# Kernel optimization log

Hardware: AMD Instinct MI355X
Metric: run time of the kernel (lower is better)

## Reference

```python
import jax, jax.numpy as jnp
import numpy as np

D = 512
H = 8
HD = D // H

def setup_inputs() -> dict:
    key = jax.random.key(0)
    ks = jax.random.split(key, 16)
    B, L = 8, 384
    s = 1.0 / np.sqrt(D)
    inp = {
        "hidden_states": jax.random.normal(ks[0], (B, L, D), jnp.float32),
        "position_embeddings": jax.random.normal(ks[1], (L, L, D), jnp.float32),
        "attention_mask": jnp.ones((B, L), jnp.int32),
        "ln_g": jnp.ones((D,), jnp.float32),
        "ln_b": jnp.zeros((D,), jnp.float32),
        "Wq": jax.random.normal(ks[2], (D, D), jnp.float32) * s,
        "bq": jnp.zeros((D,), jnp.float32),
        "Wk": jax.random.normal(ks[3], (D, D), jnp.float32) * s,
        "bk": jnp.zeros((D,), jnp.float32),
        "Wv": jax.random.normal(ks[4], (D, D), jnp.float32) * s,
        "bv": jnp.zeros((D,), jnp.float32),
        "Wpos": jax.random.normal(ks[5], (D, D), jnp.float32) * s,
        "pos_bias_u": jax.random.normal(ks[6], (H, HD), jnp.float32) * 0.02,
        "pos_bias_v": jax.random.normal(ks[7], (H, HD), jnp.float32) * 0.02,
        "Wo": jax.random.normal(ks[8], (D, D), jnp.float32) * s,
        "bo": jnp.zeros((D,), jnp.float32),
    }
    return inp

def _layernorm(x, g, b, eps=1e-5):
    mu = jnp.mean(x, axis=-1, keepdims=True)
    var = jnp.var(x, axis=-1, keepdims=True)
    return (x - mu) * jax.lax.rsqrt(var + eps) * g + b

def reference(hidden_states, position_embeddings, attention_mask,
              ln_g, ln_b, Wq, bq, Wk, bk, Wv, bv, Wpos,
              pos_bias_u, pos_bias_v, Wo, bo):
    B, L, _ = hidden_states.shape
    x = _layernorm(hidden_states, ln_g, ln_b)
    # projections -> (B, L, H, HD)
    q = (x @ Wq.T + bq).reshape(B, L, H, HD)
    k = (x @ Wk.T + bk).reshape(B, L, H, HD)
    v = (x @ Wv.T + bv).reshape(B, L, H, HD)
    # relative position projection -> (H, L, L, HD); pos[h, i, j, d]
    pos = (position_embeddings @ Wpos.T).reshape(L, L, H, HD)
    pos = jnp.transpose(pos, (2, 0, 1, 3))
    q_u = q + pos_bias_u  # (B, L, H, HD)
    q_v = q + pos_bias_v
    # content score: ac[b,h,i,j] = sum_d q_u[b,i,h,d] * k[b,j,h,d]
    scores_ac = jnp.einsum('bihd,bjhd->bhij', q_u, k)
    # positional score (torch broadcast semantics): bd[b,h,i,j] = sum_d q_v[b,j,h,d] * pos[h,i,j,d]
    scores_bd = jnp.einsum('bjhd,hijd->bhij', q_v, pos)
    scores = (scores_ac + scores_bd) / np.sqrt(HD)
    mask = attention_mask[:, None, None, :]  # (B,1,1,L)
    scores = jnp.where(mask == 0, jnp.finfo(scores.dtype).min, scores)
    probs = jax.nn.softmax(scores, axis=-1)
    ctx = jnp.einsum('bhij,bjhd->bihd', probs, v).reshape(B, L, D)
    return ctx @ Wo.T + bo
```

## Files before the change

### kernel.cpp

```cpp
#include <hip/hip_runtime.h>
#include <hip/hip_bf16.h>

#define DEV __device__ __forceinline__

typedef short short8 __attribute__((ext_vector_type(8)));
typedef float f32x4 __attribute__((ext_vector_type(4)));
typedef unsigned short ushort4v __attribute__((ext_vector_type(4)));
typedef unsigned short u16;

DEV u16 f2b(float x){ __hip_bfloat16 h = __float2bfloat16(x); u16 u; __builtin_memcpy(&u, &h, 2); return u; }

DEV int swz(int row, int cb){ return row*128 + (cb ^ ((row & 7) << 4)); }
DEV int swz768(int row, int byte_in_row){ return row*768 + (byte_in_row ^ ((row & 7) << 4)); }

DEV short8 ldfrag(const u16* s, int row, int kbf){
  return *(const short8*)((const char*)s + swz(row, kbf*2));
}
DEV void st16(u16* s, int row, int cb, short8 v){
  *(short8*)((char*)s + swz(row, cb)) = v;
}
DEV f32x4 MFMA(short8 a, short8 b, f32x4 c){
  return __builtin_amdgcn_mfma_f32_16x16x32_bf16(a, b, c, 0, 0, 0);
}

template<int R>
DEV void stage_bf16(u16* lds, const u16* g, size_t rstride, int tid){
  #pragma unroll
  for (int c = tid; c < R*8; c += 256){
    int row = c >> 3, k = c & 7;
    short8 v = *(const short8*)(g + (size_t)row*rstride + k*8);
    st16(lds, row, k*16, v);
  }
}

template<int R>
DEV void stage_f32(u16* lds, const float* g, size_t rstride, int tid){
  #pragma unroll
  for (int c = tid; c < R*8; c += 256){
    int row = c >> 3, k = c & 7;
    const float* p = g + (size_t)row*rstride + k*8;
    f32x4 f0 = *(const f32x4*)p;
    f32x4 f1 = *(const f32x4*)(p + 4);
    short8 v;
    #pragma unroll
    for (int t = 0; t < 4; ++t){ v[t] = (short)f2b(f0[t]); v[t+4] = (short)f2b(f1[t]); }
    st16(lds, row, k*16, v);
  }
}

template<int MI, int NI>
DEV void mma_step(const u16* As, int ar0, const u16* Bs, int br0, f32x4 (&acc)[MI][NI], int lane){
  int r = lane & 15, kb = (lane >> 4) * 8;
  #pragma unroll
  for (int kk = 0; kk < 64; kk += 32){
    short8 a[MI], b[NI];
    #pragma unroll
    for (int mi = 0; mi < MI; ++mi) a[mi] = ldfrag(As, ar0 + mi*16 + r, kk + kb);
    #pragma unroll
    for (int ni = 0; ni < NI; ++ni) b[ni] = ldfrag(Bs, br0 + ni*16 + r, kk + kb);
    #pragma unroll
    for (int mi = 0; mi < MI; ++mi)
      #pragma unroll
      for (int ni = 0; ni < NI; ++ni)
        acc[mi][ni] = MFMA(a[mi], b[ni], acc[mi][ni]);
  }
}

__global__ __launch_bounds__(256) void k_ln(const float* __restrict__ hs, const float* __restrict__ g,
                                            const float* __restrict__ bb, u16* __restrict__ xbf){
  int lane = threadIdx.x & 63, wid = threadIdx.x >> 6;
  int row = blockIdx.x * 4 + wid;
  const float* p = hs + (size_t)row * 512;
  f32x4 v0 = ((const f32x4*)p)[lane];
  f32x4 v1 = ((const f32x4*)p)[lane + 64];
  float s = 0.f, s2 = 0.f;
  #pragma unroll
  for (int t = 0; t < 4; ++t){ s += v0[t] + v1[t]; s2 += v0[t]*v0[t] + v1[t]*v1[t]; }
  #pragma unroll
  for (int off = 32; off; off >>= 1){ s += __shfl_xor(s, off); s2 += __shfl_xor(s2, off); }
  float mu = s * (1.0f/512.0f);
  float var = s2 * (1.0f/512.0f) - mu*mu;
  float rs = rsqrtf(var + 1e-5f);
  int e0 = lane * 4, e1 = 256 + e0;
  ushort4v o0, o1;
  #pragma unroll
  for (int t = 0; t < 4; ++t){
    o0[t] = f2b((v0[t]-mu)*rs*g[e0+t]+bb[e0+t]);
    o1[t] = f2b((v1[t]-mu)*rs*g[e1+t]+bb[e1+t]);
  }
  *(ushort4v*)(xbf + (size_t)row*512 + e0) = o0;
  *(ushort4v*)(xbf + (size_t)row*512 + e1) = o1;
}

__global__ __launch_bounds__(256) void k_wpt(const float* __restrict__ Wpos, u16* __restrict__ Wpt){
  int idx = blockIdx.x * 256 + threadIdx.x;
  int o = idx >> 9, e = idx & 511;
  int h = o >> 6, d = o & 63;
  Wpt[((size_t)h*512 + e)*64 + d] = f2b(Wpos[idx]);
}

__global__ __launch_bounds__(256) void k_qkv(const u16* __restrict__ xbf,
    const float* __restrict__ Wq, const float* __restrict__ Wk, const float* __restrict__ Wv,
    const float* __restrict__ bq, const float* __restrict__ bk, const float* __restrict__ bv,
    const float* __restrict__ pbu, const float* __restrict__ pbv,
    u16* __restrict__ qu, u16* __restrict__ qv, u16* __restrict__ kkb, u16* __restrict__ vt){
  __shared__ __align__(16) u16 As[128*64];
  __shared__ __align__(16) u16 Bs[128*64];
  int tid = threadIdx.x, lane = tid & 63, wid = tid >> 6;
  int t0 = blockIdx.x * 128, n0 = blockIdx.y * 128, z = blockIdx.z;
  const float* W    = (z==0) ? Wq : (z==1) ? Wk : Wv;
  const float* bias = (z==0) ? bq : (z==1) ? bk : bv;
  f32x4 acc[4][4] = {};
  for (int k0 = 0; k0 < 512; k0 += 64){
    stage_bf16<128>(As, xbf + (size_t)t0*512 + k0, 512, tid);
    stage_f32<128>(Bs, W + (size_t)n0*512 + k0, 512, tid);
    __syncthreads();
    mma_step<4,4>(As, (wid>>1)*64, Bs, (wid&1)*64, acc, lane);
    __syncthreads();
  }
  int r = lane & 15, half = lane >> 4;
  #pragma unroll
  for (int mi = 0; mi < 4; ++mi)
  #pragma unroll
  for (int ni = 0; ni < 4; ++ni){
    int n = n0 + (wid&1)*64 + ni*16 + r;
    int h = n >> 6, d = n & 63;
    int m0 = t0 + (wid>>1)*64 + mi*16 + half*4;
    #pragma unroll
    for (int q = 0; q < 4; ++q){
      int t = m0 + q, b = t / 384, i = t - b*384;
      float v = acc[mi][ni][q] + bias[n];
      if (z == 0){
        qu[((size_t)(b*8+h)*384 + i)*64 + d] = f2b(v + pbu[n]);
        qv[((size_t)h*3072 + t)*64 + d]      = f2b(v + pbv[n]);
      } else if (z == 1){
        kkb[((size_t)(b*8+h)*384 + i)*64 + d] = f2b(v);
      } else {
        vt[((size_t)(b*8+h)*64 + d)*384 + i] = f2b(v);
      }
    }
  }
}

__global__ __launch_bounds__(256) void k_qw(const u16* __restrict__ qv, const u16* __restrict__ Wpt,
                                            u16* __restrict__ qW){
  __shared__ __align__(16) u16 As[128*64];
  __shared__ __align__(16) u16 Bs[128*64];
  int tid = threadIdx.x, lane = tid & 63, wid = tid >> 6;
  int t0 = blockIdx.x * 128, e0 = blockIdx.y * 128, h = blockIdx.z;
  f32x4 acc[4][4] = {};
  stage_bf16<128>(As, qv + ((size_t)h*3072 + t0)*64, 64, tid);
  stage_bf16<128>(Bs, Wpt + ((size_t)h*512 + e0)*64, 64, tid);
  __syncthreads();
  mma_step<4,4>(As, (wid>>1)*64, Bs, (wid&1)*64, acc, lane);
  int r = lane & 15, half = lane >> 4;
  #pragma unroll
  for (int mi = 0; mi < 4; ++mi)
  #pragma unroll
  for (int ni = 0; ni < 4; ++ni){
    int e = e0 + (wid&1)*64 + ni*16 + r;
    int m0 = t0 + (wid>>1)*64 + mi*16 + half*4;
    #pragma unroll
    for (int q = 0; q < 4; ++q){
      int t = m0 + q, b = t / 384, j = t - b*384;
      int bh = b*8 + h;
      qW[((size_t)bh*384 + j)*512 + e] = f2b(acc[mi][ni][q]);
    }
  }
}

__global__ __launch_bounds__(256) void k_bd(const u16* __restrict__ qW, const float* __restrict__ P,
                                            float* __restrict__ Sbd){
  __shared__ __align__(16) u16 As[64*64];
  __shared__ __align__(16) u16 Bs[192*64];
  int tid = threadIdx.x, lane = tid & 63, wid = tid >> 6;
  int j = blockIdx.x, ib = blockIdx.y * 192;
  const u16*  Ag = qW + (size_t)j*512;
  const float* Bg = P + ((size_t)ib*384 + j)*512;
  short8 ar[2];
  f32x4  br[6][2];
  f32x4 acc[4][3] = {};

  #pragma unroll
  for (int s = 0; s < 2; ++s){ int c = tid + s*256;
    ar[s] = *(const short8*)(Ag + (size_t)(c>>3)*(384*512) + (c&7)*8); }
  #pragma unroll
  for (int s = 0; s < 6; ++s){ int c = tid + s*256;
    const float* p = Bg + (size_t)(c>>3)*(384*512) + (c&7)*8;
    br[s][0] = *(const f32x4*)p; br[s][1] = *(const f32x4*)(p+4); }

  #pragma unroll
  for (int k0 = 0; k0 < 512; k0 += 64){
    #pragma unroll
    for (int s = 0; s < 2; ++s){ int c = tid + s*256; st16(As, c>>3, (c&7)*16, ar[s]); }
    #pragma unroll
    for (int s = 0; s < 6; ++s){ int c = tid + s*256;
      short8 v;
      #pragma unroll
      for (int t = 0; t < 4; ++t){ v[t] = (short)f2b(br[s][0][t]); v[t+4] = (short)f2b(br[s][1][t]); }
      st16(Bs, c>>3, (c&7)*16, v); }
    if (k0 + 64 < 512){
      #pragma unroll
      for (int s = 0; s < 2; ++s){ int c = tid + s*256;
        ar[s] = *(const short8*)(Ag + (size_t)(c>>3)*(384*512) + (k0+64) + (c&7)*8); }
      #pragma unroll
      for (int s = 0; s < 6; ++s){ int c = tid + s*256;
        const float* p = Bg + (size_t)(c>>3)*(384*512) + (k0+64) + (c&7)*8;
        br[s][0] = *(const f32x4*)p; br[s][1] = *(const f32x4*)(p+4); }
    }
    __syncthreads();
    mma_step<4,3>(As, 0, Bs, wid*48, acc, lane);
    __syncthreads();
  }
  int r = lane & 15, half = lane >> 4;
  #pragma unroll
  for (int mi = 0; mi < 4; ++mi)
  #pragma unroll
  for (int ni = 0; ni < 3; ++ni){
    int i = ib + wid*48 + ni*16 + r;
    #pragma unroll
    for (int q = 0; q < 4; ++q){
      int bh = mi*16 + half*4 + q;
      Sbd[((size_t)j*64 + bh)*384 + i] = acc[mi][ni][q];
    }
  }
}

__global__ __launch_bounds__(256) void k_fin(const u16* __restrict__ qu, const u16* __restrict__ kkb,
                                             const u16* __restrict__ vt, const float* __restrict__ Sbd,
                                             const int* __restrict__ mask, u16* __restrict__ ctx){
  __shared__ __align__(16) char lds[72*1024];
  __shared__ float smbuf[2][4][2][16];
  u16* Ks = (u16*)lds;
  u16* Qs = (u16*)(lds + 48*1024);
  u16* Ps = (u16*)lds;
  u16* Vs = (u16*)(lds + 24*1024);
  int tid = threadIdx.x, lane = tid & 63, wid = tid >> 6;
  int r = lane & 15, half = lane >> 4;
  int i0 = blockIdx.x * 32, bh = blockIdx.y, b = bh >> 3, h = bh & 7;

  stage_bf16<384>(Ks, kkb + (size_t)bh*384*64, 64, tid);
  stage_bf16<32>(Qs, qu + ((size_t)bh*384 + i0)*64, 64, tid);
  __syncthreads();

  f32x4 acc[6][2] = {};
  mma_step<6,2>(Ks, wid*96, Qs, 0, acc, lane);

  int jw = wid*96 + half*4;
  #pragma unroll
  for (int mi = 0; mi < 6; ++mi){
    #pragma unroll
    for (int q = 0; q < 4; ++q){
      int j = jw + mi*16 + q;
      bool dead = (mask[b*384 + j] == 0);
      const float* srow = Sbd + ((size_t)j*64 + bh)*384 + i0;
      #pragma unroll
      for (int ni = 0; ni < 2; ++ni){
        float v = (acc[mi][ni][q] + srow[ni*16 + r]) * 0.125f;
        acc[mi][ni][q] = dead ? -3.402823466e38f : v;
      }
    }
  }

  short8 vreg[12];
  #pragma unroll
  for (int c = 0; c < 12; ++c){
    int cc = tid + c*256;
    int d = cc / 48, jc = cc - d*48;
    vreg[c] = *(const short8*)(vt + ((size_t)bh*64 + d)*384 + jc*8);
  }

  float mx[2];
  #pragma unroll
  for (int ni = 0; ni < 2; ++ni){
    float m = -3.402823466e38f;
    #pragma unroll
    for (int mi = 0; mi < 6; ++mi){
      f32x4 a = acc[mi][ni];
      m = fmaxf(m, fmaxf(fmaxf(a[0],a[1]), fmaxf(a[2],a[3])));
    }
    m = fmaxf(m, __shfl_xor(m, 16));
    m = fmaxf(m, __shfl_xor(m, 32));
    mx[ni] = m;
  }
  if (lane < 16){ smbuf[0][wid][0][r] = mx[0]; smbuf[0][wid][1][r] = mx[1]; }
  __syncthreads();
  #pragma unroll
  for (int ni = 0; ni < 2; ++ni)
    mx[ni] = fmaxf(fmaxf(smbuf[0][0][ni][r], smbuf[0][1][ni][r]),
                   fmaxf(smbuf[0][2][ni][r], smbuf[0][3][ni][r]));

  float sum[2] = {0.f, 0.f};
  #pragma unroll
  for (int ni = 0; ni < 2; ++ni){
    #pragma unroll
    for (int mi = 0; mi < 6; ++mi)
      #pragma unroll
      for (int q = 0; q < 4; ++q){
        float e = __expf(acc[mi][ni][q] - mx[ni]);
        acc[mi][ni][q] = e; sum[ni] += e;
      }
    sum[ni] += __shfl_xor(sum[ni], 16);
    sum[ni] += __shfl_xor(sum[ni], 32);
  }
  if (lane < 16){ smbuf[1][wid][0][r] = sum[0]; smbuf[1][wid][1][r] = sum[1]; }
  __syncthreads();
  float inv[2];
  #pragma unroll
  for (int ni = 0; ni < 2; ++ni)
    inv[ni] = 1.0f / (smbuf[1][0][ni][r] + smbuf[1][1][ni][r] + smbuf[1][2][ni][r] + smbuf[1][3][ni][r]);

  #pragma unroll
  for (int mi = 0; mi < 6; ++mi){
    int jb = jw + mi*16;
    #pragma unroll
    for (int ni = 0; ni < 2; ++ni){
      int i = ni*16 + r;
      ushort4v pk;
      #pragma unroll
      for (int q = 0; q < 4; ++q) pk[q] = f2b(acc[mi][ni][q] * inv[ni]);
      *(ushort4v*)((char*)Ps + swz768(i, jb*2)) = pk;
    }
  }
  #pragma unroll
  for (int c = 0; c < 12; ++c){
    int cc = tid + c*256;
    int d = cc / 48, jc = cc - d*48;
    *(short8*)((char*)Vs + swz768(d, jc*16)) = vreg[c];
  }
  __syncthreads();

  f32x4 acc2[2] = {};
  #pragma unroll
  for (int ks = 0; ks < 384; ks += 32){
    int j0 = ks + half*8;
    short8 bfr = *(const short8*)((const char*)Vs + swz768(wid*16 + r, j0*2));
    #pragma unroll
    for (int mi = 0; mi < 2; ++mi){
      short8 afr = *(const short8*)((const char*)Ps + swz768(mi*16 + r, j0*2));
      acc2[mi] = MFMA(afr, bfr, acc2[mi]);
    }
  }
  #pragma unroll
  for (int mi = 0; mi < 2; ++mi)
    #pragma unroll
    for (int q = 0; q < 4; ++q){
      int i = i0 + mi*16 + half*4 + q;
      int d = wid*16 + r;
      ctx[((size_t)(b*384 + i))*512 + h*64 + d] = f2b(acc2[mi][q]);
    }
}

__global__ __launch_bounds__(256) void k_out(const u16* __restrict__ ctx, const float* __restrict__ Wo,
                                             const float* __restrict__ bo, float* __restrict__ out){
  __shared__ __align__(16) u16 As[128*64];
  __shared__ __align__(16) u16 Bs[128*64];
  int tid = threadIdx.x, lane = tid & 63, wid = tid >> 6;
  int t0 = blockIdx.x * 128, n0 = blockIdx.y * 128;
  f32x4 acc[4][4] = {};
  for (int k0 = 0; k0 < 512; k0 += 64){
    stage_bf16<128>(As, ctx + (size_t)t0*512 + k0, 512, tid);
    stage_f32<128>(Bs, Wo + (size_t)n0*512 + k0, 512, tid);
    __syncthreads();
    mma_step<4,4>(As, (wid>>1)*64, Bs, (wid&1)*64, acc, lane);
    __syncthreads();
  }
  int r = lane & 15, half = lane >> 4;
  #pragma unroll
  for (int mi = 0; mi < 4; ++mi)
  #pragma unroll
  for (int ni = 0; ni < 4; ++ni){
    int n = n0 + (wid&1)*64 + ni*16 + r;
    int m0 = t0 + (wid>>1)*64 + mi*16 + half*4;
    #pragma unroll
    for (int q = 0; q < 4; ++q){
      int t = m0 + q;
      out[(size_t)t*512 + n] = acc[mi][ni][q] + bo[n];
    }
  }
}

extern "C" void kernel_launch(void* const* d_in, const int* in_sizes, int n_in,
                              void* d_out, int out_size, void* d_ws, size_t ws_size,
                              hipStream_t stream) {
  const float* hs   = (const float*)d_in[0];
  const float* P    = (const float*)d_in[1];
  const int*   mask = (const int*)d_in[2];
  const float* ln_g = (const float*)d_in[3];
  const float* ln_b = (const float*)d_in[4];
  const float* Wq   = (const float*)d_in[5];
  const float* bq   = (const float*)d_in[6];
  const float* Wk   = (const float*)d_in[7];
  const float* bk   = (const float*)d_in[8];
  const float* Wv   = (const float*)d_in[9];
  const float* bv   = (const float*)d_in[10];
  const float* Wpos = (const float*)d_in[11];
  const float* pbu  = (const float*)d_in[12];
  const float* pbv  = (const float*)d_in[13];
  const float* Wo   = (const float*)d_in[14];
  const float* bo   = (const float*)d_in[15];
  float* out = (float*)d_out;

  char* w = (char*)d_ws;
  u16* xbf = (u16*)w;   w += (size_t)3072*512*2;
  u16* qu  = (u16*)w;   w += (size_t)3072*512*2;
  u16* qv  = (u16*)w;   w += (size_t)3072*512*2;
  u16* kkb = (u16*)w;   w += (size_t)3072*512*2;
  u16* vt  = (u16*)w;   w += (size_t)3072*512*2;
  u16* Wpt = (u16*)w;   w += (size_t)8*512*64*2;
  u16* ctx = (u16*)w;   w += (size_t)3072*512*2;
  u16* qW  = (u16*)w;   w += (size_t)64*384*512*2;
  float* Sbd = (float*)w; w += (size_t)64*384*384*4;

  k_ln <<<768, 256, 0, stream>>>(hs, ln_g, ln_b, xbf);
  k_wpt<<<1024, 256, 0, stream>>>(Wpos, Wpt);
  k_qkv<<<dim3(24,4,3), 256, 0, stream>>>(xbf, Wq, Wk, Wv, bq, bk, bv, pbu, pbv, qu, qv, kkb, vt);
  k_qw <<<dim3(24,4,8), 256, 0, stream>>>(qv, Wpt, qW);
  k_bd <<<dim3(384,2), 256, 0, stream>>>(qW, P, Sbd);
  k_fin<<<dim3(12,64), 256, 0, stream>>>(qu, kkb, vt, Sbd, mask, ctx);
  k_out<<<dim3(24,4), 256, 0, stream>>>(ctx, Wo, bo, out);
}
```

Before: 197.1 us.

## Load P fragments directly into registers in k_bd, staging only qW in LDS

The k_bd kernel now reads the fp32 position-embedding tile straight from global memory into MFMA B-fragment registers and converts it to bf16 in place, instead of staging it through shared memory. Only the qW A-operand is staged, in two halves of 256 along K, and the loop is restructured into larger K chunks with fewer barriers. The grid is swapped so that the two i-blocks sharing a j run adjacently, and launch bounds request 3 blocks per SIMD. The aim is to cut LDS traffic and synchronisation on the dominant P stream, at the cost of less coalesced per-lane global loads and no explicit prefetch.

```diff
diff --git a/kernel.cpp b/kernel.cpp
--- a/kernel.cpp
+++ b/kernel.cpp
@@ -169,50 +169,54 @@
   }
 }
 
-__global__ __launch_bounds__(256) void k_bd(const u16* __restrict__ qW, const float* __restrict__ P,
-                                            float* __restrict__ Sbd){
-  __shared__ __align__(16) u16 As[64*64];
-  __shared__ __align__(16) u16 Bs[192*64];
+__global__ __launch_bounds__(256, 3) void k_bd(const u16* __restrict__ qW, const float* __restrict__ P,
+                                               float* __restrict__ Sbd){
+  __shared__ __align__(16) u16 As[64*256];
   int tid = threadIdx.x, lane = tid & 63, wid = tid >> 6;
-  int j = blockIdx.x, ib = blockIdx.y * 192;
-  const u16*  Ag = qW + (size_t)j*512;
-  const float* Bg = P + ((size_t)ib*384 + j)*512;
-  short8 ar[2];
-  f32x4  br[6][2];
+  int r = lane & 15, half = lane >> 4;
+  int ib = blockIdx.x * 192, j = blockIdx.y;
+
+  const float* Bp[3];
+  #pragma unroll
+  for (int ni = 0; ni < 3; ++ni){
+    int i = ib + wid*48 + ni*16 + r;
+    Bp[ni] = P + ((size_t)i*384 + j)*512 + half*8;
+  }
+  const u16* Ag = qW + (size_t)j*512;
+
   f32x4 acc[4][3] = {};
-
-  #pragma unroll
-  for (int s = 0; s < 2; ++s){ int c = tid + s*256;
-    ar[s] = *(const short8*)(Ag + (size_t)(c>>3)*(384*512) + (c&7)*8); }
-  #pragma unroll
-  for (int s = 0; s < 6; ++s){ int c = tid + s*256;
-    const float* p = Bg + (size_t)(c>>3)*(384*512) + (c&7)*8;
-    br[s][0] = *(const f32x4*)p; br[s][1] = *(const f32x4*)(p+4); }
-
-  #pragma unroll
-  for (int k0 = 0; k0 < 512; k0 += 64){
-    #pragma unroll
-    for (int s = 0; s < 2; ++s){ int c = tid + s*256; st16(As, c>>3, (c&7)*16, ar[s]); }
-    #pragma unroll
-    for (int s = 0; s < 6; ++s){ int c = tid + s*256;
-      short8 v;
-      #pragma unroll
-      for (int t = 0; t < 4; ++t){ v[t] = (short)f2b(br[s][0][t]); v[t+4] = (short)f2b(br[s][1][t]); }
-      st16(Bs, c>>3, (c&7)*16, v); }
-    if (k0 + 64 < 512){
-      #pragma unroll
-      for (int s = 0; s < 2; ++s){ int c = tid + s*256;
-        ar[s] = *(const short8*)(Ag + (size_t)(c>>3)*(384*512) + (k0+64) + (c&7)*8); }
-      #pragma unroll
-      for (int s = 0; s < 6; ++s){ int c = tid + s*256;
-        const float* p = Bg + (size_t)(c>>3)*(384*512) + (k0+64) + (c&7)*8;
-        br[s][0] = *(const f32x4*)p; br[s][1] = *(const f32x4*)(p+4); }
+  #pragma unroll
+  for (int kh = 0; kh < 2; ++kh){
+    if (kh) __syncthreads();
+    #pragma unroll
+    for (int s = 0; s < 8; ++s){
+      int c = tid + s*256;
+      int bh = c >> 5, c16 = c & 31;
+      short8 v = *(const short8*)(Ag + (size_t)bh*(384*512) + kh*256 + c16*8);
+      *(short8*)((char*)As + bh*512 + ((c16*16) ^ ((bh & 7) << 4))) = v;
     }
     __syncthreads();
-    mma_step<4,3>(As, 0, Bs, wid*48, acc, lane);
-    __syncthreads();
-  }
-  int r = lane & 15, half = lane >> 4;
+    #pragma unroll
+    for (int k32 = 0; k32 < 8; ++k32){
+      int e0 = kh*256 + k32*32;
+      short8 bfr[3];
+      #pragma unroll
+      for (int ni = 0; ni < 3; ++ni){
+        f32x4 f0 = *(const f32x4*)(Bp[ni] + e0);
+        f32x4 f1 = *(const f32x4*)(Bp[ni] + e0 + 4);
+        #pragma unroll
+        for (int t = 0; t < 4; ++t){ bfr[ni][t] = (short)f2b(f0[t]); bfr[ni][t+4] = (short)f2b(f1[t]); }
+      }
+      #pragma unroll
+      for (int mi = 0; mi < 4; ++mi){
+        int row = mi*16 + r;
+        short8 afr = *(const short8*)((const char*)As + row*512 + ((k32*64 + half*16) ^ ((row & 7) << 4)));
+        #pragma unroll
+        for (int ni = 0; ni < 3; ++ni)
+          acc[mi][ni] = MFMA(afr, bfr[ni], acc[mi][ni]);
+      }
+    }
+  }
   #pragma unroll
   for (int mi = 0; mi < 4; ++mi)
   #pragma unroll
@@ -416,7 +420,7 @@
   k_wpt<<<1024, 256, 0, stream>>>(Wpos, Wpt);
   k_qkv<<<dim3(24,4,3), 256, 0, stream>>>(xbf, Wq, Wk, Wv, bq, bk, bv, pbu, pbv, qu, qv, kkb, vt);
   k_qw <<<dim3(24,4,8), 256, 0, stream>>>(qv, Wpt, qW);
-  k_bd <<<dim3(384,2), 256, 0, stream>>>(qW, P, Sbd);
+  k_bd <<<dim3(2,384), 256, 0, stream>>>(qW, P, Sbd);
   k_fin<<<dim3(12,64), 256, 0, stream>>>(qu, kkb, vt, Sbd, mask, ctx);
   k_out<<<dim3(24,4), 256, 0, stream>>>(ctx, Wo, bo, out);
 }
```

Measured after the change: 196.0 us. Within noise of the previous version (-0.6%).
